# Kernel tuning notes

Hardware: AMD Instinct MI355X
Metric: run time of the kernel (lower is better)

Reference implementation:

```python
import jax, jax.numpy as jnp
import numpy as np

ALPHA = 0.2        # LeakyReLU slope for attention scores (init arg alpha)
MLP_ALPHA = 0.01   # torch nn.LeakyReLU default slope in aftermlp
EPS = 1e-5         # nn.LayerNorm default eps


def leaky(x, a):
    return jnp.where(x >= 0, x, a * x)


def setup_inputs() -> dict:
    key = jax.random.key(0)
    ks = jax.random.split(key, 12)
    B, N, FIN, FOUT, K = 4, 4096, 256, 256, 64
    s = 0.05
    return {
        "h": jax.random.normal(ks[0], (B, N, FIN), jnp.float32),
        "adj": jax.random.uniform(ks[1], (B, N, N), jnp.float32),
        "W": jax.random.normal(ks[2], (FIN, FOUT), jnp.float32) * s,
        "a": jax.random.normal(ks[3], (FOUT, 1), jnp.float32) * s,
        "ln_g": jnp.ones((FOUT,), jnp.float32),
        "ln_b": jnp.zeros((FOUT,), jnp.float32),
        "W1": jax.random.normal(ks[4], (FOUT, FOUT), jnp.float32) * s,
        "b1": jnp.zeros((FOUT,), jnp.float32),
        "W2": jax.random.normal(ks[5], (FOUT, FOUT), jnp.float32) * s,
        "b2": jnp.zeros((FOUT,), jnp.float32),
        "W3": jax.random.normal(ks[6], (FOUT, FOUT), jnp.float32) * s,
        "b3": jnp.zeros((FOUT,), jnp.float32),
        "k": K,
    }


def reference(h, adj, W, a, ln_g, ln_b, W1, b1, W2, b2, W3, b3, k):
    # Wh: [B, N, F]
    Wh = h @ W
    B, N, Fd = Wh.shape
    C = N // k
    Whc = Wh.reshape(B, C, k, Fd)                       # [B, C, k, F]
    # a_input[b,c,i,j] = Wh[b,c,i]  =>  e[b,c,i,j] = leaky(Wh[b,c,i] . a)
    e = leaky(jnp.squeeze(Whc @ a, -1), ALPHA)          # [B, C, k]
    # block-diagonal chunks of adj: [B, C, k, k]
    idx = jnp.arange(C)
    blocks = adj.reshape(B, C, k, C, k)[:, idx, :, idx, :]  # [C, B, k, k]
    blocks = jnp.transpose(blocks, (1, 0, 2, 3))            # [B, C, k, k]
    scores = jax.nn.softmax(blocks * e[..., :, None], axis=-1)  # [B, C, k, k]
    out = jnp.einsum('bcij,bcjf->bcif', scores, Whc)    # [B, C, k, F]
    # aftermlp: Linear -> LeakyReLU(0.01) -> Linear -> LeakyReLU(0.01) -> Linear
    y = leaky(out @ W1 + b1, MLP_ALPHA)
    y = leaky(y @ W2 + b2, MLP_ALPHA)
    y = y @ W3 + b3
    # residual + LayerNorm over last dim
    z = y + out
    mu = jnp.mean(z, axis=-1, keepdims=True)
    var = jnp.var(z, axis=-1, keepdims=True)
    z = (z - mu) / jnp.sqrt(var + EPS) * ln_g + ln_b
    return z.reshape(B, N, Fd)
```

## Files before the change

### kernel.cpp

```cpp
#include <hip/hip_runtime.h>

typedef __bf16 bf16;
typedef __bf16 bf16x4 __attribute__((ext_vector_type(4)));
typedef __bf16 bf16x8 __attribute__((ext_vector_type(8)));
typedef float  f32x4  __attribute__((ext_vector_type(4)));

#define ALPHA 0.2f
#define MLP_ALPHA 0.01f
#define LN_EPS 1e-5f

constexpr int Bb = 4;
constexpr int Nn = 4096;
constexpr int Ff = 256;
constexpr int Kk = 64;
constexpr int Cc = 64;

__device__ __forceinline__ f32x4 MFMA(bf16x8 a, bf16x8 b, f32x4 c) {
  return __builtin_amdgcn_mfma_f32_16x16x32_bf16(a, b, c, 0, 0, 0);
}
__device__ __forceinline__ bf16x4 pack4(f32x4 v) {
  bf16x4 r; r[0]=(bf16)v[0]; r[1]=(bf16)v[1]; r[2]=(bf16)v[2]; r[3]=(bf16)v[3]; return r;
}

__global__ __launch_bounds__(256) void prep_weights(
    const float* __restrict__ W0, const float* __restrict__ W1,
    const float* __restrict__ W2, const float* __restrict__ W3,
    bf16* __restrict__ outw)
{
  int t = blockIdx.x * 256 + threadIdx.x;
  int l   = t & 63;
  int nt  = (t >> 6) & 15;
  int kt  = (t >> 10) & 7;
  int mat = t >> 13;
  const float* src = (mat==0) ? W0 : (mat==1) ? W1 : (mat==2) ? W2 : W3;
  int n  = nt*16 + (l & 15);
  int k0 = kt*32 + (l >> 4)*8;
  bf16x8 v;
  #pragma unroll
  for (int jj = 0; jj < 8; ++jj) v[jj] = (bf16)src[(k0 + jj)*Ff + n];
  *(bf16x8*)(outw + (size_t)t * 8) = v;
}

__device__ __forceinline__ void mlp_gemm(const bf16* __restrict__ wfrag, int mat,
                                         const bf16* inBuf, f32x4 acc[4][4],
                                         int w, int l)
{
  const int g = l >> 4, li = l & 15;
  #pragma unroll 2
  for (int kt = 0; kt < 8; ++kt) {
    bf16x8 af[4], bfr[4];
    #pragma unroll
    for (int r = 0; r < 4; ++r) {
      const bf16* p = wfrag + ((((size_t)mat*8 + kt)*16 + (w*4 + r))*64 + l)*8;
      af[r] = *(const bf16x8*)p;
    }
    #pragma unroll
    for (int nt = 0; nt < 4; ++nt) {
      int i = nt*16 + li;
      int byte = i*512 + (((kt*32 + g*8)*2) ^ ((i & 7) << 4));
      bfr[nt] = *(const bf16x8*)((const char*)inBuf + byte);
    }
    #pragma unroll
    for (int nt = 0; nt < 4; ++nt)
      #pragma unroll
      for (int r = 0; r < 4; ++r)
        acc[nt][r] = MFMA(af[r], bfr[nt], acc[nt][r]);
  }
}

__device__ __forceinline__ void stage_store(f32x4 acc[4][4], const float* __restrict__ bias,
                                            bf16* outBuf, int w, int l)
{
  const int g = l >> 4, li = l & 15;
  float bv[4][4];
  #pragma unroll
  for (int r = 0; r < 4; ++r)
    #pragma unroll
    for (int e = 0; e < 4; ++e) bv[r][e] = bias[(w*4 + r)*16 + g*4 + e];
  #pragma unroll
  for (int nt = 0; nt < 4; ++nt) {
    int i = nt*16 + li, swz = (i & 7) << 4;
    #pragma unroll
    for (int r = 0; r < 4; ++r) {
      f32x4 v;
      #pragma unroll
      for (int e = 0; e < 4; ++e) {
        float x = acc[nt][r][e] + bv[r][e];
        v[e] = (x >= 0.f) ? x : MLP_ALPHA * x;
      }
      int f0 = (w*4 + r)*16 + g*4;
      *(bf16x4*)((char*)outBuf + i*512 + ((f0*2) ^ swz)) = pack4(v);
    }
  }
}

__global__ __launch_bounds__(256, 1) void gat_mfma(
    const float* __restrict__ h,   const float* __restrict__ adj,
    const float* __restrict__ a_vec,
    const float* __restrict__ gln, const float* __restrict__ bln,
    const float* __restrict__ b1,  const float* __restrict__ b2,
    const float* __restrict__ b3,
    const bf16* __restrict__ wfrag,
    float* __restrict__ out)
{
  __shared__ bf16 bufA[Ff * Kk];
  __shared__ bf16 bufB[Kk * Ff];
  __shared__ bf16 sS[Kk * Kk];
  __shared__ float lnS[Kk * 4], lnQ[Kk * 4];

  const int t = threadIdx.x, l = t & 63, w = t >> 6, g = l >> 4, li = l & 15;
  const int bc = blockIdx.x, b = bc >> 6, c = bc & 63;
  const size_t rbase = (size_t)b * Nn + c * Kk;

  float adjv[16];
  #pragma unroll
  for (int rr = 0; rr < 16; ++rr)
    adjv[rr] = adj[(rbase + w*16 + rr) * Nn + (size_t)c*Kk + l];

  f32x4 acc1[4][4];
  #pragma unroll
  for (int q = 0; q < 4; ++q)
    #pragma unroll
    for (int r = 0; r < 4; ++r) acc1[q][r] = (f32x4){0.f, 0.f, 0.f, 0.f};

  #pragma unroll 2
  for (int kt = 0; kt < 8; ++kt) {
    bf16x8 af[4];
    #pragma unroll
    for (int rt = 0; rt < 4; ++rt) {
      const float* hp = h + (rbase + rt*16 + li)*Ff + kt*32 + g*8;
      f32x4 h0 = *(const f32x4*)hp;
      f32x4 h1 = *(const f32x4*)(hp + 4);
      bf16x8 v;
      #pragma unroll
      for (int d = 0; d < 4; ++d) { v[d] = (bf16)h0[d]; v[4+d] = (bf16)h1[d]; }
      af[rt] = v;
    }
    #pragma unroll
    for (int q = 0; q < 4; ++q) {
      const bf16* p = wfrag + (((size_t)kt*16 + (w*4 + q))*64 + l)*8;
      bf16x8 bfr = *(const bf16x8*)p;
      #pragma unroll
      for (int rt = 0; rt < 4; ++rt) acc1[q][rt] = MFMA(af[rt], bfr, acc1[q][rt]);
    }
  }
  #pragma unroll
  for (int q = 0; q < 4; ++q) {
    int f = w*64 + q*16 + li, swz = (f & 7) << 4;
    #pragma unroll
    for (int rt = 0; rt < 4; ++rt) {
      int j0 = rt*16 + g*4;
      *(bf16x4*)((char*)bufA + f*128 + ((j0*2) ^ swz)) = pack4(acc1[q][rt]);
    }
  }
  __syncthreads();

  {
    float afs[4];
    #pragma unroll
    for (int q = 0; q < 4; ++q) afs[q] = a_vec[q*64 + l];
    #pragma unroll
    for (int rr = 0; rr < 16; ++rr) {
      int i = w*16 + rr;
      float p = 0.f;
      #pragma unroll
      for (int q = 0; q < 4; ++q) {
        int f = q*64 + l;
        int byte = f*128 + ((i*2) ^ ((f & 7) << 4));
        p += (float)(*(const bf16*)((const char*)bufA + byte)) * afs[q];
      }
      #pragma unroll
      for (int off = 32; off; off >>= 1) p += __shfl_xor(p, off);
      float e = (p >= 0.f) ? p : ALPHA * p;
      float x = adjv[rr] * e;
      float m = x;
      #pragma unroll
      for (int off = 32; off; off >>= 1) m = fmaxf(m, __shfl_xor(m, off));
      float pe = __expf(x - m);
      float s = pe;
      #pragma unroll
      for (int off = 32; off; off >>= 1) s += __shfl_xor(s, off);
      float sv = pe / s;
      int byte = i*128 + ((l*2) ^ ((i & 7) << 4));
      *(bf16*)((char*)sS + byte) = (bf16)sv;
    }
  }
  __syncthreads();

  f32x4 xr[4][4];
  #pragma unroll
  for (int nt = 0; nt < 4; ++nt)
    #pragma unroll
    for (int r = 0; r < 4; ++r) xr[nt][r] = (f32x4){0.f, 0.f, 0.f, 0.f};
  #pragma unroll
  for (int kt = 0; kt < 2; ++kt) {
    int koff = (kt*32 + g*8) * 2;
    bf16x8 af[4], bfr[4];
    #pragma unroll
    for (int r = 0; r < 4; ++r) {
      int f = (w*4 + r)*16 + li;
      af[r] = *(const bf16x8*)((const char*)bufA + f*128 + (koff ^ ((f & 7) << 4)));
    }
    #pragma unroll
    for (int nt = 0; nt < 4; ++nt) {
      int i = nt*16 + li;
      bfr[nt] = *(const bf16x8*)((const char*)sS + i*128 + (koff ^ ((i & 7) << 4)));
    }
    #pragma unroll
    for (int nt = 0; nt < 4; ++nt)
      #pragma unroll
      for (int r = 0; r < 4; ++r) xr[nt][r] = MFMA(af[r], bfr[nt], xr[nt][r]);
  }
  #pragma unroll
  for (int nt = 0; nt < 4; ++nt) {
    int i = nt*16 + li, swz = (i & 7) << 4;
    #pragma unroll
    for (int r = 0; r < 4; ++r) {
      int f0 = (w*4 + r)*16 + g*4;
      *(bf16x4*)((char*)bufB + i*512 + ((f0*2) ^ swz)) = pack4(xr[nt][r]);
    }
  }
  __syncthreads();

  f32x4 acc3[4][4];
  #pragma unroll
  for (int nt = 0; nt < 4; ++nt)
    #pragma unroll
    for (int r = 0; r < 4; ++r) acc3[nt][r] = (f32x4){0.f, 0.f, 0.f, 0.f};
  mlp_gemm(wfrag, 1, bufB, acc3, w, l);
  stage_store(acc3, b1, bufA, w, l);
  __syncthreads();

  #pragma unroll
  for (int nt = 0; nt < 4; ++nt)
    #pragma unroll
    for (int r = 0; r < 4; ++r) acc3[nt][r] = (f32x4){0.f, 0.f, 0.f, 0.f};
  mlp_gemm(wfrag, 2, bufA, acc3, w, l);
  stage_store(acc3, b2, bufB, w, l);
  __syncthreads();

  #pragma unroll
  for (int nt = 0; nt < 4; ++nt)
    #pragma unroll
    for (int r = 0; r < 4; ++r) acc3[nt][r] = (f32x4){0.f, 0.f, 0.f, 0.f};
  mlp_gemm(wfrag, 3, bufB, acc3, w, l);

  {
    float bv[4][4], gv[4][4], btv[4][4];
    #pragma unroll
    for (int r = 0; r < 4; ++r)
      #pragma unroll
      for (int e = 0; e < 4; ++e) {
        int f = (w*4 + r)*16 + g*4 + e;
        bv[r][e] = b3[f]; gv[r][e] = gln[f]; btv[r][e] = bln[f];
      }
    float ps[4], pq[4];
    #pragma unroll
    for (int nt = 0; nt < 4; ++nt) {
      float s = 0.f, qq = 0.f;
      #pragma unroll
      for (int r = 0; r < 4; ++r)
        #pragma unroll
        for (int e = 0; e < 4; ++e) {
          float z = acc3[nt][r][e] + bv[r][e] + xr[nt][r][e];
          acc3[nt][r][e] = z;
          s += z; qq += z*z;
        }
      s  += __shfl_xor(s, 16);  s  += __shfl_xor(s, 32);
      qq += __shfl_xor(qq, 16); qq += __shfl_xor(qq, 32);
      ps[nt] = s; pq[nt] = qq;
    }
    if (g == 0) {
      #pragma unroll
      for (int nt = 0; nt < 4; ++nt) {
        int i = nt*16 + li;
        lnS[i*4 + w] = ps[nt];
        lnQ[i*4 + w] = pq[nt];
      }
    }
    __syncthreads();
    #pragma unroll
    for (int nt = 0; nt < 4; ++nt) {
      int i = nt*16 + li;
      f32x4 s4 = *(const f32x4*)&lnS[i*4];
      f32x4 q4 = *(const f32x4*)&lnQ[i*4];
      float s  = s4[0] + s4[1] + s4[2] + s4[3];
      float qq = q4[0] + q4[1] + q4[2] + q4[3];
      float mu  = s * (1.f/256.f);
      float var = qq * (1.f/256.f) - mu*mu;
      float rs  = rsqrtf(var + LN_EPS);
      #pragma unroll
      for (int r = 0; r < 4; ++r) {
        float4 o;
        o.x = (acc3[nt][r][0] - mu)*rs*gv[r][0] + btv[r][0];
        o.y = (acc3[nt][r][1] - mu)*rs*gv[r][1] + btv[r][1];
        o.z = (acc3[nt][r][2] - mu)*rs*gv[r][2] + btv[r][2];
        o.w = (acc3[nt][r][3] - mu)*rs*gv[r][3] + btv[r][3];
        *(float4*)&out[(rbase + i)*Ff + (w*4 + r)*16 + g*4] = o;
      }
    }
  }
}

extern "C" void kernel_launch(void* const* d_in, const int* in_sizes, int n_in,
                              void* d_out, int out_size, void* d_ws, size_t ws_size,
                              hipStream_t stream) {
  (void)in_sizes; (void)n_in; (void)out_size; (void)ws_size;
  bf16* wfrag = (bf16*)d_ws;
  prep_weights<<<dim3(128), dim3(256), 0, stream>>>(
      (const float*)d_in[2], (const float*)d_in[6],
      (const float*)d_in[8], (const float*)d_in[10], wfrag);
  gat_mfma<<<dim3(Bb * Cc), dim3(256), 0, stream>>>(
      (const float*)d_in[0],  (const float*)d_in[1],  (const float*)d_in[3],
      (const float*)d_in[4],  (const float*)d_in[5],
      (const float*)d_in[7],  (const float*)d_in[9],  (const float*)d_in[11],
      wfrag, (float*)d_out);
}
```

Before: 44.32 us.

## Use 512 threads per block, precompute W·a, stage h in LDS

```diff
diff --git a/kernel.cpp b/kernel.cpp
--- a/kernel.cpp
+++ b/kernel.cpp
@@ -21,17 +21,29 @@
 __device__ __forceinline__ bf16x4 pack4(f32x4 v) {
   bf16x4 r; r[0]=(bf16)v[0]; r[1]=(bf16)v[1]; r[2]=(bf16)v[2]; r[3]=(bf16)v[3]; return r;
 }
+__device__ __forceinline__ int swz512(int i, int inrow) { return i*512 + (inrow ^ ((i & 15) << 4)); }
+__device__ __forceinline__ int swz128(int f, int inrow) { return f*128 + (inrow ^ ((f & 7) << 4)); }
 
 __global__ __launch_bounds__(256) void prep_weights(
     const float* __restrict__ W0, const float* __restrict__ W1,
     const float* __restrict__ W2, const float* __restrict__ W3,
-    bf16* __restrict__ outw)
+    const float* __restrict__ a_vec,
+    bf16* __restrict__ outw, float* __restrict__ wa)
 {
+  if (blockIdx.x == 128) {
+    int k = threadIdx.x;
+    const float* row = W0 + k * Ff;
+    float s = 0.f;
+    for (int j = 0; j < Ff; j += 4) {
+      f32x4 wv = *(const f32x4*)(row + j);
+      f32x4 av = *(const f32x4*)(a_vec + j);
+      s += wv[0]*av[0] + wv[1]*av[1] + wv[2]*av[2] + wv[3]*av[3];
+    }
+    wa[k] = s;
+    return;
+  }
   int t = blockIdx.x * 256 + threadIdx.x;
-  int l   = t & 63;
-  int nt  = (t >> 6) & 15;
-  int kt  = (t >> 10) & 7;
-  int mat = t >> 13;
+  int l = t & 63, nt = (t >> 6) & 15, kt = (t >> 10) & 7, mat = t >> 13;
   const float* src = (mat==0) ? W0 : (mat==1) ? W1 : (mat==2) ? W2 : W3;
   int n  = nt*16 + (l & 15);
   int k0 = kt*32 + (l >> 4)*8;
@@ -42,191 +54,187 @@
 }
 
 __device__ __forceinline__ void mlp_gemm(const bf16* __restrict__ wfrag, int mat,
-                                         const bf16* inBuf, f32x4 acc[4][4],
+                                         const bf16* inBuf, f32x4 acc[4][2],
                                          int w, int l)
 {
   const int g = l >> 4, li = l & 15;
-  #pragma unroll 2
+  #pragma unroll
   for (int kt = 0; kt < 8; ++kt) {
-    bf16x8 af[4], bfr[4];
-    #pragma unroll
-    for (int r = 0; r < 4; ++r) {
-      const bf16* p = wfrag + ((((size_t)mat*8 + kt)*16 + (w*4 + r))*64 + l)*8;
-      af[r] = *(const bf16x8*)p;
-    }
+    bf16x8 af[2], bfr[4];
+    #pragma unroll
+    for (int r = 0; r < 2; ++r)
+      af[r] = *(const bf16x8*)(wfrag + ((((size_t)mat*8 + kt)*16 + (w*2 + r))*64 + l)*8);
     #pragma unroll
     for (int nt = 0; nt < 4; ++nt) {
       int i = nt*16 + li;
-      int byte = i*512 + (((kt*32 + g*8)*2) ^ ((i & 7) << 4));
-      bfr[nt] = *(const bf16x8*)((const char*)inBuf + byte);
+      bfr[nt] = *(const bf16x8*)((const char*)inBuf + swz512(i, (kt*32 + g*8)*2));
     }
     #pragma unroll
     for (int nt = 0; nt < 4; ++nt)
       #pragma unroll
-      for (int r = 0; r < 4; ++r)
+      for (int r = 0; r < 2; ++r)
         acc[nt][r] = MFMA(af[r], bfr[nt], acc[nt][r]);
   }
 }
 
-__device__ __forceinline__ void stage_store(f32x4 acc[4][4], const float* __restrict__ bias,
+__device__ __forceinline__ void stage_store(f32x4 acc[4][2], const float* __restrict__ bias,
                                             bf16* outBuf, int w, int l)
 {
   const int g = l >> 4, li = l & 15;
-  float bv[4][4];
-  #pragma unroll
-  for (int r = 0; r < 4; ++r)
-    #pragma unroll
-    for (int e = 0; e < 4; ++e) bv[r][e] = bias[(w*4 + r)*16 + g*4 + e];
+  float bv[2][4];
+  #pragma unroll
+  for (int r = 0; r < 2; ++r)
+    #pragma unroll
+    for (int e = 0; e < 4; ++e) bv[r][e] = bias[(w*2 + r)*16 + g*4 + e];
   #pragma unroll
   for (int nt = 0; nt < 4; ++nt) {
-    int i = nt*16 + li, swz = (i & 7) << 4;
-    #pragma unroll
-    for (int r = 0; r < 4; ++r) {
+    int i = nt*16 + li;
+    #pragma unroll
+    for (int r = 0; r < 2; ++r) {
       f32x4 v;
       #pragma unroll
       for (int e = 0; e < 4; ++e) {
         float x = acc[nt][r][e] + bv[r][e];
         v[e] = (x >= 0.f) ? x : MLP_ALPHA * x;
       }
-      int f0 = (w*4 + r)*16 + g*4;
-      *(bf16x4*)((char*)outBuf + i*512 + ((f0*2) ^ swz)) = pack4(v);
-    }
-  }
-}
-
-__global__ __launch_bounds__(256, 1) void gat_mfma(
+      int f0 = (w*2 + r)*16 + g*4;
+      *(bf16x4*)((char*)outBuf + swz512(i, f0*2)) = pack4(v);
+    }
+  }
+}
+
+__global__ __launch_bounds__(512, 2) void gat_mfma(
     const float* __restrict__ h,   const float* __restrict__ adj,
-    const float* __restrict__ a_vec,
     const float* __restrict__ gln, const float* __restrict__ bln,
     const float* __restrict__ b1,  const float* __restrict__ b2,
     const float* __restrict__ b3,
-    const bf16* __restrict__ wfrag,
+    const bf16* __restrict__ wfrag, const float* __restrict__ wa,
     float* __restrict__ out)
 {
+  __shared__ bf16 hbs[Kk * Ff];
   __shared__ bf16 bufA[Ff * Kk];
   __shared__ bf16 bufB[Kk * Ff];
   __shared__ bf16 sS[Kk * Kk];
-  __shared__ float lnS[Kk * 4], lnQ[Kk * 4];
+  __shared__ float evec[Kk];
+  __shared__ float lnS[Kk * 8], lnQ[Kk * 8];
 
   const int t = threadIdx.x, l = t & 63, w = t >> 6, g = l >> 4, li = l & 15;
   const int bc = blockIdx.x, b = bc >> 6, c = bc & 63;
   const size_t rbase = (size_t)b * Nn + c * Kk;
 
-  float adjv[16];
-  #pragma unroll
-  for (int rr = 0; rr < 16; ++rr)
-    adjv[rr] = adj[(rbase + w*16 + rr) * Nn + (size_t)c*Kk + l];
-
-  f32x4 acc1[4][4];
-  #pragma unroll
-  for (int q = 0; q < 4; ++q)
-    #pragma unroll
-    for (int r = 0; r < 4; ++r) acc1[q][r] = (f32x4){0.f, 0.f, 0.f, 0.f};
-
-  #pragma unroll 2
+  float adjv[8];
+  #pragma unroll
+  for (int rr = 0; rr < 8; ++rr)
+    adjv[rr] = adj[(rbase + w*8 + rr) * Nn + (size_t)c*Kk + l];
+
+  {
+    const int i  = t >> 3;
+    const int k0 = (t & 7) * 32;
+    const float* hp = h + (rbase + i) * Ff + k0;
+    float p = 0.f;
+    #pragma unroll
+    for (int u = 0; u < 4; ++u) {
+      f32x4 h0 = *(const f32x4*)(hp + u*8);
+      f32x4 h1 = *(const f32x4*)(hp + u*8 + 4);
+      f32x4 w0 = *(const f32x4*)(wa + k0 + u*8);
+      f32x4 w1 = *(const f32x4*)(wa + k0 + u*8 + 4);
+      p += h0[0]*w0[0] + h0[1]*w0[1] + h0[2]*w0[2] + h0[3]*w0[3]
+         + h1[0]*w1[0] + h1[1]*w1[1] + h1[2]*w1[2] + h1[3]*w1[3];
+      bf16x8 v;
+      #pragma unroll
+      for (int d = 0; d < 4; ++d) { v[d] = (bf16)h0[d]; v[4+d] = (bf16)h1[d]; }
+      *(bf16x8*)((char*)hbs + swz512(i, (k0 + u*8)*2)) = v;
+    }
+    p += __shfl_xor(p, 1); p += __shfl_xor(p, 2); p += __shfl_xor(p, 4);
+    if ((l & 7) == 0) evec[i] = (p >= 0.f) ? p : ALPHA * p;
+  }
+  __syncthreads();
+
+  #pragma unroll
+  for (int rr = 0; rr < 8; ++rr) {
+    int i = w*8 + rr;
+    float x = adjv[rr] * evec[i];
+    float m = x;
+    #pragma unroll
+    for (int off = 32; off; off >>= 1) m = fmaxf(m, __shfl_xor(m, off));
+    float pe = __expf(x - m);
+    float s = pe;
+    #pragma unroll
+    for (int off = 32; off; off >>= 1) s += __shfl_xor(s, off);
+    *(bf16*)((char*)sS + swz128(i, l*2)) = (bf16)(pe / s);
+  }
+
+  f32x4 acc1[2][4];
+  #pragma unroll
+  for (int q = 0; q < 2; ++q)
+    #pragma unroll
+    for (int rt = 0; rt < 4; ++rt) acc1[q][rt] = (f32x4){0.f,0.f,0.f,0.f};
+  #pragma unroll
   for (int kt = 0; kt < 8; ++kt) {
     bf16x8 af[4];
     #pragma unroll
     for (int rt = 0; rt < 4; ++rt) {
-      const float* hp = h + (rbase + rt*16 + li)*Ff + kt*32 + g*8;
-      f32x4 h0 = *(const f32x4*)hp;
-      f32x4 h1 = *(const f32x4*)(hp + 4);
-      bf16x8 v;
-      #pragma unroll
-      for (int d = 0; d < 4; ++d) { v[d] = (bf16)h0[d]; v[4+d] = (bf16)h1[d]; }
-      af[rt] = v;
-    }
-    #pragma unroll
-    for (int q = 0; q < 4; ++q) {
-      const bf16* p = wfrag + (((size_t)kt*16 + (w*4 + q))*64 + l)*8;
-      bf16x8 bfr = *(const bf16x8*)p;
+      int i = rt*16 + li;
+      af[rt] = *(const bf16x8*)((const char*)hbs + swz512(i, (kt*32 + g*8)*2));
+    }
+    #pragma unroll
+    for (int q = 0; q < 2; ++q) {
+      bf16x8 bfr = *(const bf16x8*)(wfrag + (((size_t)kt*16 + (w*2 + q))*64 + l)*8);
       #pragma unroll
       for (int rt = 0; rt < 4; ++rt) acc1[q][rt] = MFMA(af[rt], bfr, acc1[q][rt]);
     }
   }
   #pragma unroll
-  for (int q = 0; q < 4; ++q) {
-    int f = w*64 + q*16 + li, swz = (f & 7) << 4;
+  for (int q = 0; q < 2; ++q) {
+    int f = (w*2 + q)*16 + li;
     #pragma unroll
     for (int rt = 0; rt < 4; ++rt) {
       int j0 = rt*16 + g*4;
-      *(bf16x4*)((char*)bufA + f*128 + ((j0*2) ^ swz)) = pack4(acc1[q][rt]);
-    }
-  }
-  __syncthreads();
-
-  {
-    float afs[4];
-    #pragma unroll
-    for (int q = 0; q < 4; ++q) afs[q] = a_vec[q*64 + l];
-    #pragma unroll
-    for (int rr = 0; rr < 16; ++rr) {
-      int i = w*16 + rr;
-      float p = 0.f;
-      #pragma unroll
-      for (int q = 0; q < 4; ++q) {
-        int f = q*64 + l;
-        int byte = f*128 + ((i*2) ^ ((f & 7) << 4));
-        p += (float)(*(const bf16*)((const char*)bufA + byte)) * afs[q];
-      }
-      #pragma unroll
-      for (int off = 32; off; off >>= 1) p += __shfl_xor(p, off);
-      float e = (p >= 0.f) ? p : ALPHA * p;
-      float x = adjv[rr] * e;
-      float m = x;
-      #pragma unroll
-      for (int off = 32; off; off >>= 1) m = fmaxf(m, __shfl_xor(m, off));
-      float pe = __expf(x - m);
-      float s = pe;
-      #pragma unroll
-      for (int off = 32; off; off >>= 1) s += __shfl_xor(s, off);
-      float sv = pe / s;
-      int byte = i*128 + ((l*2) ^ ((i & 7) << 4));
-      *(bf16*)((char*)sS + byte) = (bf16)sv;
-    }
-  }
-  __syncthreads();
-
-  f32x4 xr[4][4];
+      *(bf16x4*)((char*)bufA + swz128(f, j0*2)) = pack4(acc1[q][rt]);
+    }
+  }
+  __syncthreads();
+
+  f32x4 xr[4][2];
   #pragma unroll
   for (int nt = 0; nt < 4; ++nt)
     #pragma unroll
-    for (int r = 0; r < 4; ++r) xr[nt][r] = (f32x4){0.f, 0.f, 0.f, 0.f};
+    for (int r = 0; r < 2; ++r) xr[nt][r] = (f32x4){0.f,0.f,0.f,0.f};
   #pragma unroll
   for (int kt = 0; kt < 2; ++kt) {
-    int koff = (kt*32 + g*8) * 2;
-    bf16x8 af[4], bfr[4];
-    #pragma unroll
-    for (int r = 0; r < 4; ++r) {
-      int f = (w*4 + r)*16 + li;
-      af[r] = *(const bf16x8*)((const char*)bufA + f*128 + (koff ^ ((f & 7) << 4)));
+    int koff = (kt*32 + g*8)*2;
+    bf16x8 af[2], bfr[4];
+    #pragma unroll
+    for (int r = 0; r < 2; ++r) {
+      int f = (w*2 + r)*16 + li;
+      af[r] = *(const bf16x8*)((const char*)bufA + swz128(f, koff));
     }
     #pragma unroll
     for (int nt = 0; nt < 4; ++nt) {
       int i = nt*16 + li;
-      bfr[nt] = *(const bf16x8*)((const char*)sS + i*128 + (koff ^ ((i & 7) << 4)));
+      bfr[nt] = *(const bf16x8*)((const char*)sS + swz128(i, koff));
     }
     #pragma unroll
     for (int nt = 0; nt < 4; ++nt)
       #pragma unroll
-      for (int r = 0; r < 4; ++r) xr[nt][r] = MFMA(af[r], bfr[nt], xr[nt][r]);
+      for (int r = 0; r < 2; ++r) xr[nt][r] = MFMA(af[r], bfr[nt], xr[nt][r]);
   }
   #pragma unroll
   for (int nt = 0; nt < 4; ++nt) {
-    int i = nt*16 + li, swz = (i & 7) << 4;
-    #pragma unroll
-    for (int r = 0; r < 4; ++r) {
-      int f0 = (w*4 + r)*16 + g*4;
-      *(bf16x4*)((char*)bufB + i*512 + ((f0*2) ^ swz)) = pack4(xr[nt][r]);
-    }
-  }
-  __syncthreads();
-
-  f32x4 acc3[4][4];
+    int i = nt*16 + li;
+    #pragma unroll
+    for (int r = 0; r < 2; ++r) {
+      int f0 = (w*2 + r)*16 + g*4;
+      *(bf16x4*)((char*)bufB + swz512(i, f0*2)) = pack4(xr[nt][r]);
+    }
+  }
+  __syncthreads();
+
+  f32x4 acc3[4][2];
   #pragma unroll
   for (int nt = 0; nt < 4; ++nt)
     #pragma unroll
-    for (int r = 0; r < 4; ++r) acc3[nt][r] = (f32x4){0.f, 0.f, 0.f, 0.f};
+    for (int r = 0; r < 2; ++r) acc3[nt][r] = (f32x4){0.f,0.f,0.f,0.f};
   mlp_gemm(wfrag, 1, bufB, acc3, w, l);
   stage_store(acc3, b1, bufA, w, l);
   __syncthreads();
@@ -234,7 +242,7 @@
   #pragma unroll
   for (int nt = 0; nt < 4; ++nt)
     #pragma unroll
-    for (int r = 0; r < 4; ++r) acc3[nt][r] = (f32x4){0.f, 0.f, 0.f, 0.f};
+    for (int r = 0; r < 2; ++r) acc3[nt][r] = (f32x4){0.f,0.f,0.f,0.f};
   mlp_gemm(wfrag, 2, bufA, acc3, w, l);
   stage_store(acc3, b2, bufB, w, l);
   __syncthreads();
@@ -242,24 +250,23 @@
   #pragma unroll
   for (int nt = 0; nt < 4; ++nt)
     #pragma unroll
-    for (int r = 0; r < 4; ++r) acc3[nt][r] = (f32x4){0.f, 0.f, 0.f, 0.f};
+    for (int r = 0; r < 2; ++r) acc3[nt][r] = (f32x4){0.f,0.f,0.f,0.f};
   mlp_gemm(wfrag, 3, bufB, acc3, w, l);
 
   {
-    float bv[4][4], gv[4][4], btv[4][4];
-    #pragma unroll
-    for (int r = 0; r < 4; ++r)
+    float bv[2][4], gv[2][4], btv[2][4];
+    #pragma unroll
+    for (int r = 0; r < 2; ++r)
       #pragma unroll
       for (int e = 0; e < 4; ++e) {
-        int f = (w*4 + r)*16 + g*4 + e;
+        int f = (w*2 + r)*16 + g*4 + e;
         bv[r][e] = b3[f]; gv[r][e] = gln[f]; btv[r][e] = bln[f];
       }
-    float ps[4], pq[4];
     #pragma unroll
     for (int nt = 0; nt < 4; ++nt) {
       float s = 0.f, qq = 0.f;
       #pragma unroll
-      for (int r = 0; r < 4; ++r)
+      for (int r = 0; r < 2; ++r)
         #pragma unroll
         for (int e = 0; e < 4; ++e) {
           float z = acc3[nt][r][e] + bv[r][e] + xr[nt][r][e];
@@ -268,35 +275,33 @@
         }
       s  += __shfl_xor(s, 16);  s  += __shfl_xor(s, 32);
       qq += __shfl_xor(qq, 16); qq += __shfl_xor(qq, 32);
-      ps[nt] = s; pq[nt] = qq;
-    }
-    if (g == 0) {
-      #pragma unroll
-      for (int nt = 0; nt < 4; ++nt) {
+      if (g == 0) {
         int i = nt*16 + li;
-        lnS[i*4 + w] = ps[nt];
-        lnQ[i*4 + w] = pq[nt];
+        lnS[i*8 + w] = s;
+        lnQ[i*8 + w] = qq;
       }
     }
     __syncthreads();
     #pragma unroll
     for (int nt = 0; nt < 4; ++nt) {
       int i = nt*16 + li;
-      f32x4 s4 = *(const f32x4*)&lnS[i*4];
-      f32x4 q4 = *(const f32x4*)&lnQ[i*4];
-      float s  = s4[0] + s4[1] + s4[2] + s4[3];
-      float qq = q4[0] + q4[1] + q4[2] + q4[3];
+      f32x4 s0 = *(const f32x4*)&lnS[i*8];
+      f32x4 s1 = *(const f32x4*)&lnS[i*8 + 4];
+      f32x4 q0 = *(const f32x4*)&lnQ[i*8];
+      f32x4 q1 = *(const f32x4*)&lnQ[i*8 + 4];
+      float s  = s0[0]+s0[1]+s0[2]+s0[3]+s1[0]+s1[1]+s1[2]+s1[3];
+      float qq = q0[0]+q0[1]+q0[2]+q0[3]+q1[0]+q1[1]+q1[2]+q1[3];
       float mu  = s * (1.f/256.f);
       float var = qq * (1.f/256.f) - mu*mu;
       float rs  = rsqrtf(var + LN_EPS);
       #pragma unroll
-      for (int r = 0; r < 4; ++r) {
+      for (int r = 0; r < 2; ++r) {
         float4 o;
         o.x = (acc3[nt][r][0] - mu)*rs*gv[r][0] + btv[r][0];
         o.y = (acc3[nt][r][1] - mu)*rs*gv[r][1] + btv[r][1];
         o.z = (acc3[nt][r][2] - mu)*rs*gv[r][2] + btv[r][2];
         o.w = (acc3[nt][r][3] - mu)*rs*gv[r][3] + btv[r][3];
-        *(float4*)&out[(rbase + i)*Ff + (w*4 + r)*16 + g*4] = o;
+        *(float4*)&out[(rbase + i)*Ff + (w*2 + r)*16 + g*4] = o;
       }
     }
   }
@@ -306,13 +311,15 @@
                               void* d_out, int out_size, void* d_ws, size_t ws_size,
                               hipStream_t stream) {
   (void)in_sizes; (void)n_in; (void)out_size; (void)ws_size;
-  bf16* wfrag = (bf16*)d_ws;
-  prep_weights<<<dim3(128), dim3(256), 0, stream>>>(
+  bf16*  wfrag = (bf16*)d_ws;
+  float* wa    = (float*)((char*)d_ws + 512*1024);
+  prep_weights<<<dim3(129), dim3(256), 0, stream>>>(
       (const float*)d_in[2], (const float*)d_in[6],
-      (const float*)d_in[8], (const float*)d_in[10], wfrag);
-  gat_mfma<<<dim3(Bb * Cc), dim3(256), 0, stream>>>(
-      (const float*)d_in[0],  (const float*)d_in[1],  (const float*)d_in[3],
+      (const float*)d_in[8], (const float*)d_in[10],
+      (const float*)d_in[3], wfrag, wa);
+  gat_mfma<<<dim3(Bb * Cc), dim3(512), 0, stream>>>(
+      (const float*)d_in[0],  (const float*)d_in[1],
       (const float*)d_in[4],  (const float*)d_in[5],
       (const float*)d_in[7],  (const float*)d_in[9],  (const float*)d_in[11],
-      wfrag, (float*)d_out);
-}
+      wfrag, wa, (float*)d_out);
+}
```

Measured after the change: 36.82 us. -16.9%, faster.
